# Optimization experiments

Measured on AMD Instinct MI355X. Metric: run time of the kernel, lower is better.

## Reference

```python
import jax, jax.numpy as jnp
import numpy as np
from jax import lax

PRE_NMS_THRESH = 0.05
PRE_NMS_TOP_N = 1000
FINAL_NMS_THRESH = 0.4  # hardcoded in forward(): boxlist_nms(..., 0.4)
MIN_SIZE = 0
STRIDE = 4.0
NEG = -1e9

N, C, H, W = 32, 1, 384, 384


def setup_inputs() -> dict:
    key = jax.random.key(0)
    k1, k2 = jax.random.split(key)
    box_cls = jax.random.uniform(k1, (N, C, H, W), dtype=jnp.float32)
    box_regression = jax.random.normal(k2, (N, 4, H, W), dtype=jnp.float32) * 20.0
    image_sizes = jnp.full((N, 2), H * int(STRIDE), dtype=jnp.int32)
    return {"box_cls": box_cls, "box_regression": box_regression, "image_sizes": image_sizes}


def decode_boxes(quad):
    # quad: [N, 4, H, W]; EAST geometry decode at stride 4 -> xyxy
    n, _, h, w = quad.shape
    x = (jnp.arange(w, dtype=quad.dtype) * STRIDE)[None, :]   # [1, W]
    y = (jnp.arange(h, dtype=quad.dtype) * STRIDE)[:, None]   # [H, 1]
    ymin = y - quad[:, 0]
    xmax = x + quad[:, 1]
    ymax = y + quad[:, 2]
    xmin = x - quad[:, 3]
    return jnp.stack([xmin, ymin, xmax, ymax], axis=1)  # [N, 4, H, W] (permute (3,0,1,2))


def iou_matrix(b):
    # b: [K, 4] xyxy
    x1, y1, x2, y2 = b[:, 0], b[:, 1], b[:, 2], b[:, 3]
    area = jnp.clip(x2 - x1, 0) * jnp.clip(y2 - y1, 0)
    ix1 = jnp.maximum(x1[:, None], x1[None, :])
    iy1 = jnp.maximum(y1[:, None], y1[None, :])
    ix2 = jnp.minimum(x2[:, None], x2[None, :])
    iy2 = jnp.minimum(y2[:, None], y2[None, :])
    inter = jnp.clip(ix2 - ix1, 0) * jnp.clip(iy2 - iy1, 0)
    union = area[:, None] + area[None, :] - inter
    return inter / jnp.maximum(union, 1e-9)


def greedy_nms(boxes, init_keep):
    # boxes: [K, 4] sorted by descending score; init_keep: [K] bool
    K = boxes.shape[0]
    iou = iou_matrix(boxes)
    idx = jnp.arange(K)

    def body(i, keep):
        suppress = (iou[i] > FINAL_NMS_THRESH) & (idx > i)
        return jnp.where(keep[i], keep & ~suppress, keep)

    return lax.fori_loop(0, K, body, init_keep)


def _forward(box_cls, box_regression):
    n, c, h, w = box_cls.shape
    boxes = decode_boxes(box_regression)                       # [N, 4, H, W]
    boxes = boxes.transpose(0, 2, 3, 1).reshape(n, h * w, 4)   # [N, HW, 4]
    scores = box_cls.transpose(0, 2, 3, 1).reshape(n, h * w)   # [N, HW] (C=1)

    # threshold + conditional top-k (padding with NEG emulates variable counts)
    masked = jnp.where(scores > PRE_NMS_THRESH, scores, NEG)
    scores_k, idx_k = lax.top_k(masked, PRE_NMS_TOP_N)         # [N, K], sorted desc
    boxes_k = jnp.take_along_axis(boxes, idx_k[..., None], axis=1)  # [N, K, 4]

    valid = scores_k > PRE_NMS_THRESH
    ws = boxes_k[..., 2] - boxes_k[..., 0]
    hs = boxes_k[..., 3] - boxes_k[..., 1]
    valid = valid & (ws >= MIN_SIZE) & (hs >= MIN_SIZE)        # remove_small_boxes

    keep = jax.vmap(greedy_nms)(boxes_k, valid)                # [N, K]
    out = jnp.concatenate([boxes_k, scores_k[..., None]], axis=-1)
    out = out * keep[..., None].astype(out.dtype)              # [N, K, 5]
    return out, keep


def reference(box_cls, box_regression, image_sizes):
    return _forward(box_cls, box_regression)
```

## Files before the change

kernel.cpp:

```cpp
#include <hip/hip_runtime.h>
#include <stdint.h>

#define NIMG 32
#define WID 384
#define HW 147456
#define TOPK 1000
#define KPAD 1024
#define NBINS 512
#define BIN_SCALEF 512.0f
#define SEGCAP 256
#define CANDCAP 2048
#define THRESH 0.05f
#define PREF_C 0.99f
#define NMS_T 0.4f
#define NBLK 18

typedef unsigned long long u64;
typedef unsigned int u32;

#define PCNT_OFF 0
#define PCAND_OFF 4096

__device__ __forceinline__ float area_of(float x0, float y0, float x1, float y1) {
  float a = fmaxf(x1 - x0, 0.0f) * fmaxf(y1 - y0, 0.0f);
  asm volatile("" : "+v"(a));
  return a;
}

__device__ __forceinline__ bool iou_gt(float ax0, float ay0, float ax1, float ay1, float aa,
                                       float bx0, float by0, float bx1, float by1, float ba) {
  float ix1 = fmaxf(ax0, bx0);
  float iy1 = fmaxf(ay0, by0);
  float ix2 = fminf(ax1, bx1);
  float iy2 = fminf(ay1, by1);
  float iw = fmaxf(ix2 - ix1, 0.0f);
  float ih = fmaxf(iy2 - iy1, 0.0f);
  float inter = iw * ih;
  asm volatile("" : "+v"(inter));
  float uni = fmaxf(aa + ba - inter, 1e-9f);
  return (inter / uni) > NMS_T;
}

__device__ __forceinline__ u64 shflxor64(u64 v, int m) {
  int lo = __shfl_xor((int)(u32)v, m, 64);
  int hi = __shfl_xor((int)(u32)(v >> 32), m, 64);
  return ((u64)(u32)hi << 32) | (u32)lo;
}

__device__ __forceinline__ u64 make_key(float s, u32 idx) {
  u32 ord = __float_as_uint(s) | 0x80000000u;
  return ((u64)ord << 32) | (u32)(~idx);
}

__device__ __forceinline__ int bin_of(float s) {
  int b = (int)(s * BIN_SCALEF);
  return b < 0 ? 0 : (b > NBINS - 1 ? NBINS - 1 : b);
}

__global__ __launch_bounds__(256) void scan_kernel(const float* __restrict__ cls,
                                                   u32* __restrict__ pcnt,
                                                   u64* __restrict__ pcand) {
  __shared__ u64 lbuf[SEGCAP];
  __shared__ u32 lcnt;
  const int n = blockIdx.y;
  const int tid = threadIdx.x;
  const int lane = tid & 63;
  if (tid == 0) lcnt = 0;
  __syncthreads();

  const float4* src = (const float4*)(cls + (size_t)n * HW) + blockIdx.x * 2048;
  float4 A[8];
#pragma unroll
  for (int v = 0; v < 8; v++) A[v] = src[tid + v * 256];

  const u64 ltmask = (1ull << lane) - 1ull;
#pragma unroll
  for (int v = 0; v < 8; v++) {
    float ss[4] = {A[v].x, A[v].y, A[v].z, A[v].w};
#pragma unroll
    for (int c = 0; c < 4; c++) {
      float s = ss[c];
      bool pc = s > PREF_C;
      u64 m = __ballot(pc);
      if (m) {
        int ldr = __ffsll(m) - 1;
        u32 wb = 0;
        if (lane == ldr) wb = atomicAdd(&lcnt, (u32)__popcll(m));
        wb = (u32)__shfl((int)wb, ldr, 64);
        if (pc) {
          u32 pos = wb + (u32)__popcll(m & ltmask);
          if (pos < SEGCAP) lbuf[pos] = make_key(s, (u32)((blockIdx.x * 2048 + tid + v * 256) * 4 + c));
        }
      }
    }
  }
  __syncthreads();
  const int seg = n * NBLK + blockIdx.x;
  if (tid == 0) pcnt[seg] = (lcnt > SEGCAP) ? 0xFFFFFFFFu : lcnt;
  u32 c = lcnt < SEGCAP ? lcnt : (u32)SEGCAP;
  u64* pc = pcand + (size_t)seg * SEGCAP;
  for (u32 i = tid; i < c; i += 256) pc[i] = lbuf[i];
}

#define REGCHAIN(K, JSTART) do {                                            \
    const bool desc_ = ((tid & ((K) >> 1)) == 0);                           \
    for (int j_ = (JSTART); j_ >= 2; j_ >>= 1) {                            \
      int h_ = j_ >> 1;                                                     \
      bool low_ = (tid & h_) == 0;                                          \
      u64 p0_ = shflxor64(e0, h_), p1_ = shflxor64(e1, h_);                 \
      bool tm_ = (low_ == desc_);                                           \
      e0 = tm_ ? (e0 > p0_ ? e0 : p0_) : (e0 < p0_ ? e0 : p0_);             \
      e1 = tm_ ? (e1 > p1_ ? e1 : p1_) : (e1 < p1_ ? e1 : p1_);             \
    }                                                                       \
    { u64 lo_ = e0 < e1 ? e0 : e1, hi_ = e0 < e1 ? e1 : e0;                 \
      e0 = desc_ ? hi_ : lo_; e1 = desc_ ? lo_ : hi_; }                     \
  } while (0)

__global__ __launch_bounds__(1024) void fused_kernel(const float* __restrict__ cls,
                                                     const float* __restrict__ reg,
                                                     const u32* __restrict__ pcnt,
                                                     const u64* __restrict__ pcand,
                                                     float* __restrict__ out) {
  __shared__ u64 skey[CANDCAP];
  __shared__ u32 scnt[NBLK];
  __shared__ u32 soff[NBLK];
  __shared__ u32 bs[NBINS];
  __shared__ u32 stmp[64];
  __shared__ int stbin;
  __shared__ u32 sflag, sfc;
  __shared__ float4 vbox[KPAD];
  __shared__ float varea[KPAD];
  __shared__ u64 mlds[136 * 64];
  __shared__ u32 wcnt[16], woff[16];
  __shared__ int pc[136], pk[136];
  __shared__ int sV, snch, snp;
  __shared__ u64 keepsh[16], srem[16];

  const int n = blockIdx.x;
  const int tid = threadIdx.x;
  const int lane = tid & 63;
  const u64 ltmask = (1ull << lane) - 1ull;

  if (tid < NBLK) scnt[tid] = pcnt[n * NBLK + tid];
  skey[tid] = 0ull; skey[tid + 1024] = 0ull;
  if (tid == 0) sfc = 0;
  __syncthreads();
  if (tid == 0) {
    u32 f = 0, off = 0;
    for (int s = 0; s < NBLK; s++) {
      u32 c = scnt[s];
      if (c == 0xFFFFFFFFu) { f = 1; c = 0; }
      soff[s] = off; off += c;
    }
    if (off < TOPK || off > CANDCAP) f = 1;
    sflag = f;
  }
  __syncthreads();

  if (sflag == 0) {
    for (int s = 0; s < NBLK; s++) {
      u32 c = scnt[s];
      if (tid < c) skey[soff[s] + tid] = pcand[(size_t)(n * NBLK + s) * SEGCAP + tid];
    }
  } else {
    for (int i = tid; i < NBINS; i += 1024) bs[i] = 0;
    __syncthreads();
    const float* ci = cls + (size_t)n * HW;
    for (int base = 0; base < HW; base += 1024) {
      float s = ci[base + tid];
      if (s > THRESH) atomicAdd(&bs[bin_of(s)], 1u);
    }
    __syncthreads();
    if (tid < 64) {
      u32 cs = 0;
#pragma unroll
      for (int k2 = 0; k2 < 8; k2++) cs += bs[lane * 8 + k2];
      u32 s = cs;
#pragma unroll
      for (int d = 1; d < 64; d <<= 1) {
        u32 v = (u32)__shfl_down((int)s, d, 64);
        if (lane + d < 64) s += v;
      }
      stmp[lane] = s;
      u64 mask = __ballot(s >= TOPK);
      if (lane == 0) {
        int t = 0;
        if (mask) {
          int L = 63 - __clzll(mask);
          u32 acc = (L < 63) ? stmp[L + 1] : 0;
          for (int b = L * 8 + 7; b >= L * 8; b--) {
            acc += bs[b];
            if (acc >= TOPK) { t = b; break; }
          }
        }
        stbin = t;
      }
    }
    __syncthreads();
    const int t = stbin;
    for (int base = 0; base < HW; base += 1024) {
      int i = base + tid;
      float s = ci[i];
      bool p = (s > THRESH) && (bin_of(s) >= t);
      u64 m = __ballot(p);
      if (m) {
        int ldr = __ffsll(m) - 1;
        u32 wb = 0;
        if (lane == ldr) wb = atomicAdd(&sfc, (u32)__popcll(m));
        wb = (u32)__shfl((int)wb, ldr, 64);
        if (p) { u32 pos = wb + (u32)__popcll(m & ltmask); if (pos < CANDCAP) skey[pos] = make_key(s, (u32)i); }
      }
    }
  }
  __syncthreads();

  {
    u64 e0 = skey[2 * tid], e1 = skey[2 * tid + 1];
    REGCHAIN(2, 1); REGCHAIN(4, 2); REGCHAIN(8, 4); REGCHAIN(16, 8);
    REGCHAIN(32, 16); REGCHAIN(64, 32); REGCHAIN(128, 64);
    for (int k = 256; k <= CANDCAP; k <<= 1) {
      skey[2 * tid] = e0; skey[2 * tid + 1] = e1;
      __syncthreads();
      for (int j = k >> 1; j >= 128; j >>= 1) {
        int i = ((tid & ~(j - 1)) << 1) | (tid & (j - 1));
        u64 a = skey[i], b = skey[i + j];
        bool desc = ((i & k) == 0);
        if (desc ? (a < b) : (a > b)) { skey[i] = b; skey[i + j] = a; }
        __syncthreads();
      }
      e0 = skey[2 * tid]; e1 = skey[2 * tid + 1];
      REGCHAIN(k, 64);
    }
    skey[2 * tid] = e0; skey[2 * tid + 1] = e1;
    __syncthreads();
  }

  u64 key = skey[tid];
  float4 b = make_float4(0.f, 0.f, 0.f, 0.f);
  if (key != 0ull && tid < TOPK) {
    u32 idx = ~(u32)(key & 0xFFFFFFFFull);
    int iy = (int)idx / WID;
    int ix = (int)idx - iy * WID;
    float xx = (float)ix * 4.0f;
    float yy = (float)iy * 4.0f;
    const float* rb = reg + (size_t)n * 4 * HW;
    float r0 = rb[idx];
    float r1 = rb[HW + idx];
    float r2 = rb[2 * HW + idx];
    float r3 = rb[3 * HW + idx];
    b.y = yy - r0; b.z = xx + r1; b.w = yy + r2; b.x = xx - r3;
  }
  float s = __uint_as_float((u32)(key >> 32) & 0x7FFFFFFFu);

  bool vb = (tid < TOPK) && (s > THRESH) && (b.z - b.x >= 0.0f) && (b.w - b.y >= 0.0f);
  vbox[tid] = make_float4(0.f, 0.f, 0.f, 0.f);
  varea[tid] = 0.0f;
  const int w = tid >> 6;
  u64 vm = __ballot(vb);
  if (lane == 0) wcnt[w] = (u32)__popcll(vm);
  if (tid < 16) { srem[tid] = 0ull; keepsh[tid] = 0ull; }
  __syncthreads();
  if (tid == 0) {
    u32 off = 0;
    for (int i = 0; i < 16; i++) { woff[i] = off; off += wcnt[i]; }
    int V = (int)off;
    int nch = (V + 63) >> 6;
    sV = V; snch = nch; snp = nch * (nch + 1) / 2;
  }
  __syncthreads();
  const int V = sV, nch = snch, npairs = snp;

  int pos = -1;
  if (vb) {
    pos = (int)(woff[w] + (u32)__popcll(vm & ltmask));
    vbox[pos] = b;
    varea[pos] = area_of(b.x, b.y, b.z, b.w);
  }
  if (tid < npairs) {
    int p = tid, c = 0, base = 0;
    while (p >= base + (nch - c)) { base += nch - c; c++; }
    pc[tid] = c; pk[tid] = c + (p - base);
  }
  __syncthreads();

  for (int r = w; r < npairs * 64; r += 16) {
    int p = r >> 6, i = r & 63;
    int c = pc[p], k = pk[p];
    float4 rbx = vbox[k * 64 + i];
    float rarea = varea[k * 64 + i];
    float4 cbx = vbox[c * 64 + lane];
    float carea = varea[c * 64 + lane];
    bool pred = iou_gt(rbx.x, rbx.y, rbx.z, rbx.w, rarea,
                       cbx.x, cbx.y, cbx.z, cbx.w, carea);
    u64 m = __ballot(pred);
    if (lane == 0) mlds[r] = m;
  }
  __syncthreads();

  if (tid < 64) {
    for (int c = 0; c < nch; c++) {
      int pbase = c * nch - (c * (c - 1)) / 2 - c;
      u64 diag = mlds[(pbase + c) * 64 + lane];
      u64 ainit = (V >= (c + 1) * 64) ? ~0ull
                : ((V > c * 64) ? ((1ull << (V - c * 64)) - 1ull) : 0ull);
      u64 alive;
      {
        u64 a = ainit & ~srem[c];
        u32 alo2 = __builtin_amdgcn_readfirstlane((u32)a);
        u32 ahi2 = __builtin_amdgcn_readfirstlane((u32)(a >> 32));
        alive = ((u64)ahi2 << 32) | alo2;
      }
      u32 rlo = (u32)diag, rhi = (u32)(diag >> 32);
      u64 cur = alive;
      while (cur) {
        int i = __ffsll(cur) - 1;
        u32 rl = __builtin_amdgcn_readlane(rlo, i);
        u32 rh = __builtin_amdgcn_readlane(rhi, i);
        u64 rowi = ((u64)rh << 32) | rl;
        u64 lowmask = (i == 63) ? ~0ull : ((1ull << (i + 1)) - 1ull);
        rowi &= ~lowmask;
        alive &= ~rowi;
        cur &= ~rowi;
        cur &= cur - 1;
      }
      if (lane == 0) keepsh[c] = alive;
      const u64 K = alive;
      for (int k = c + 1; k < nch; k++) {
        bool sup = (mlds[(pbase + k) * 64 + lane] & K) != 0ull;
        u64 mres = __ballot(sup);
        if (lane == 0) srem[k] |= mres;
      }
    }
  }
  __syncthreads();

  u64 kb = (vb && pos >= 0) ? ((keepsh[pos >> 6] >> (pos & 63)) & 1ull) : 0ull;
  if (tid < TOPK) {
    float f = (float)kb;
    size_t ob = (size_t)n * (TOPK * 5) + (size_t)tid * 5;
    out[ob + 0] = kb ? b.x : 0.0f;
    out[ob + 1] = kb ? b.y : 0.0f;
    out[ob + 2] = kb ? b.z : 0.0f;
    out[ob + 3] = kb ? b.w : 0.0f;
    out[ob + 4] = kb ? s : 0.0f;
    out[(size_t)NIMG * TOPK * 5 + (size_t)n * TOPK + tid] = f;
  }
}

extern "C" void kernel_launch(void* const* d_in, const int* in_sizes, int n_in,
                              void* d_out, int out_size, void* d_ws, size_t ws_size,
                              hipStream_t stream) {
  const float* cls = (const float*)d_in[0];
  const float* reg = (const float*)d_in[1];
  float* out = (float*)d_out;

  uint8_t* ws = (uint8_t*)d_ws;
  u32* pcnt = (u32*)(ws + PCNT_OFF);
  u64* pcand = (u64*)(ws + PCAND_OFF);

  scan_kernel<<<dim3(NBLK, NIMG), 256, 0, stream>>>(cls, pcnt, pcand);
  fused_kernel<<<NIMG, 1024, 0, stream>>>(cls, reg, pcnt, pcand, out);
}
```

Baseline: 177.8 us.

## Replace bitonic sort of candidates with fine-bin histogram rank sort

On the fast path, the full 2048-element bitonic sort of candidate keys is replaced by a fine histogram over scores in [0.99,1). Keys are bucketed, and each key's rank is computed by counting larger keys within its own bin. The key is then scattered directly to its rank position. Shared memory is unioned into one buffer reused by the later NMS stage. The bitonic sort is kept only for the fallback path, and an extra barrier is added to protect the aliased buffer.

```diff
diff --git a/kernel.cpp b/kernel.cpp
--- a/kernel.cpp
+++ b/kernel.cpp
@@ -14,6 +14,7 @@
 #define PREF_C 0.99f
 #define NMS_T 0.4f
 #define NBLK 18
+#define FINEBINS 256
 
 typedef unsigned long long u64;
 typedef unsigned int u32;
@@ -52,9 +53,19 @@
   return ((u64)ord << 32) | (u32)(~idx);
 }
 
+__device__ __forceinline__ float score_of(u64 key) {
+  return __uint_as_float((u32)(key >> 32) & 0x7FFFFFFFu);
+}
+
 __device__ __forceinline__ int bin_of(float s) {
   int b = (int)(s * BIN_SCALEF);
   return b < 0 ? 0 : (b > NBINS - 1 ? NBINS - 1 : b);
+}
+
+__device__ __forceinline__ int finebin(u64 key) {
+  float s = score_of(key);
+  int b = (int)((s - 0.99f) * 25600.0f);
+  return b < 0 ? 0 : (b > FINEBINS - 1 ? FINEBINS - 1 : b);
 }
 
 __global__ __launch_bounds__(256) void scan_kernel(const float* __restrict__ cls,
@@ -121,16 +132,23 @@
                                                      const u32* __restrict__ pcnt,
                                                      const u64* __restrict__ pcand,
                                                      float* __restrict__ out) {
-  __shared__ u64 skey[CANDCAP];
+  __shared__ __align__(16) unsigned char smem[90112];
+  u64* CKEY   = (u64*)smem;
+  u32* BINNED = (u32*)(smem + 16384);
+  u64* RKEY   = (u64*)(smem + 24576);
+  float4* vbox  = (float4*)smem;
+  float*  varea = (float*)(smem + 16384);
+  u64*    mlds  = (u64*)(smem + 20480);
+
+  __shared__ u32 BINSTART[FINEBINS + 1];
+  __shared__ u32 HIST[FINEBINS];
   __shared__ u32 scnt[NBLK];
   __shared__ u32 soff[NBLK];
   __shared__ u32 bs[NBINS];
   __shared__ u32 stmp[64];
   __shared__ int stbin;
   __shared__ u32 sflag, sfc;
-  __shared__ float4 vbox[KPAD];
-  __shared__ float varea[KPAD];
-  __shared__ u64 mlds[136 * 64];
+  __shared__ int sC;
   __shared__ u32 wcnt[16], woff[16];
   __shared__ int pc[136], pk[136];
   __shared__ int sV, snch, snp;
@@ -139,10 +157,13 @@
   const int n = blockIdx.x;
   const int tid = threadIdx.x;
   const int lane = tid & 63;
+  const int w = tid >> 6;
   const u64 ltmask = (1ull << lane) - 1ull;
 
   if (tid < NBLK) scnt[tid] = pcnt[n * NBLK + tid];
-  skey[tid] = 0ull; skey[tid + 1024] = 0ull;
+  CKEY[tid] = 0ull; CKEY[tid + 1024] = 0ull;
+  RKEY[tid] = 0ull;
+  if (tid < FINEBINS) HIST[tid] = 0;
   if (tid == 0) sfc = 0;
   __syncthreads();
   if (tid == 0) {
@@ -153,15 +174,63 @@
       soff[s] = off; off += c;
     }
     if (off < TOPK || off > CANDCAP) f = 1;
-    sflag = f;
-  }
-  __syncthreads();
+    sflag = f; sC = (int)off;
+  }
+  __syncthreads();
+
+  u64 key;
 
   if (sflag == 0) {
-    for (int s = 0; s < NBLK; s++) {
-      u32 c = scnt[s];
-      if (tid < c) skey[soff[s] + tid] = pcand[(size_t)(n * NBLK + s) * SEGCAP + tid];
-    }
+    const int C = sC;
+    for (int seg = w; seg < NBLK; seg += 16) {
+      u32 c = scnt[seg];
+      u32 o = soff[seg];
+      const u64* src2 = pcand + (size_t)(n * NBLK + seg) * SEGCAP;
+      for (u32 i = lane; i < c; i += 64) CKEY[o + i] = src2[i];
+    }
+    __syncthreads();
+    for (int i = tid; i < C; i += 1024) atomicAdd(&HIST[finebin(CKEY[i])], 1u);
+    __syncthreads();
+    if (tid < 64) {
+      u32 h0 = HIST[lane * 4 + 0], h1 = HIST[lane * 4 + 1];
+      u32 h2 = HIST[lane * 4 + 2], h3 = HIST[lane * 4 + 3];
+      u32 t = h0 + h1 + h2 + h3;
+      u32 incl = t;
+#pragma unroll
+      for (int d = 1; d < 64; d <<= 1) {
+        u32 v = (u32)__shfl_up((int)incl, d, 64);
+        if (lane >= d) incl += v;
+      }
+      u32 base = incl - t;
+      BINSTART[lane * 4 + 0] = base;
+      BINSTART[lane * 4 + 1] = base + h0;
+      BINSTART[lane * 4 + 2] = base + h0 + h1;
+      BINSTART[lane * 4 + 3] = base + h0 + h1 + h2;
+      if (lane == 63) BINSTART[FINEBINS] = incl;
+      HIST[lane * 4 + 0] = 0; HIST[lane * 4 + 1] = 0;
+      HIST[lane * 4 + 2] = 0; HIST[lane * 4 + 3] = 0;
+    }
+    __syncthreads();
+    for (int i = tid; i < C; i += 1024) {
+      int bb = finebin(CKEY[i]);
+      u32 slot = atomicAdd(&HIST[bb], 1u);
+      BINNED[BINSTART[bb] + slot] = (u32)i;
+    }
+    __syncthreads();
+    for (int i = tid; i < C; i += 1024) {
+      u64 k = CKEY[i];
+      int bb = finebin(k);
+      u32 s0 = BINSTART[bb], s1 = BINSTART[bb + 1];
+      u32 g = 0;
+      for (u32 j = s0; j < s1; j++) {
+        u32 cj = BINNED[j];
+        if (CKEY[cj] > k) g++;
+      }
+      u32 rank = (u32)C - s1 + g;
+      if (rank < KPAD) RKEY[rank] = k;
+    }
+    __syncthreads();
+    key = RKEY[tid];
   } else {
     for (int i = tid; i < NBINS; i += 1024) bs[i] = 0;
     __syncthreads();
@@ -188,9 +257,9 @@
         if (mask) {
           int L = 63 - __clzll(mask);
           u32 acc = (L < 63) ? stmp[L + 1] : 0;
-          for (int b = L * 8 + 7; b >= L * 8; b--) {
-            acc += bs[b];
-            if (acc >= TOPK) { t = b; break; }
+          for (int bb = L * 8 + 7; bb >= L * 8; bb--) {
+            acc += bs[bb];
+            if (acc >= TOPK) { t = bb; break; }
           }
         }
         stbin = t;
@@ -208,34 +277,33 @@
         u32 wb = 0;
         if (lane == ldr) wb = atomicAdd(&sfc, (u32)__popcll(m));
         wb = (u32)__shfl((int)wb, ldr, 64);
-        if (p) { u32 pos = wb + (u32)__popcll(m & ltmask); if (pos < CANDCAP) skey[pos] = make_key(s, (u32)i); }
-      }
-    }
-  }
-  __syncthreads();
-
-  {
-    u64 e0 = skey[2 * tid], e1 = skey[2 * tid + 1];
-    REGCHAIN(2, 1); REGCHAIN(4, 2); REGCHAIN(8, 4); REGCHAIN(16, 8);
-    REGCHAIN(32, 16); REGCHAIN(64, 32); REGCHAIN(128, 64);
-    for (int k = 256; k <= CANDCAP; k <<= 1) {
-      skey[2 * tid] = e0; skey[2 * tid + 1] = e1;
+        if (p) { u32 pos = wb + (u32)__popcll(m & ltmask); if (pos < CANDCAP) CKEY[pos] = make_key(s, (u32)i); }
+      }
+    }
+    __syncthreads();
+    {
+      u64 e0 = CKEY[2 * tid], e1 = CKEY[2 * tid + 1];
+      REGCHAIN(2, 1); REGCHAIN(4, 2); REGCHAIN(8, 4); REGCHAIN(16, 8);
+      REGCHAIN(32, 16); REGCHAIN(64, 32); REGCHAIN(128, 64);
+      for (int k = 256; k <= CANDCAP; k <<= 1) {
+        CKEY[2 * tid] = e0; CKEY[2 * tid + 1] = e1;
+        __syncthreads();
+        for (int j = k >> 1; j >= 128; j >>= 1) {
+          int i = ((tid & ~(j - 1)) << 1) | (tid & (j - 1));
+          u64 a = CKEY[i], bb = CKEY[i + j];
+          bool desc = ((i & k) == 0);
+          if (desc ? (a < bb) : (a > bb)) { CKEY[i] = bb; CKEY[i + j] = a; }
+          __syncthreads();
+        }
+        e0 = CKEY[2 * tid]; e1 = CKEY[2 * tid + 1];
+        REGCHAIN(k, 64);
+      }
+      CKEY[2 * tid] = e0; CKEY[2 * tid + 1] = e1;
       __syncthreads();
-      for (int j = k >> 1; j >= 128; j >>= 1) {
-        int i = ((tid & ~(j - 1)) << 1) | (tid & (j - 1));
-        u64 a = skey[i], b = skey[i + j];
-        bool desc = ((i & k) == 0);
-        if (desc ? (a < b) : (a > b)) { skey[i] = b; skey[i + j] = a; }
-        __syncthreads();
-      }
-      e0 = skey[2 * tid]; e1 = skey[2 * tid + 1];
-      REGCHAIN(k, 64);
-    }
-    skey[2 * tid] = e0; skey[2 * tid + 1] = e1;
-    __syncthreads();
-  }
-
-  u64 key = skey[tid];
+    }
+    key = CKEY[tid];
+  }
+
   float4 b = make_float4(0.f, 0.f, 0.f, 0.f);
   if (key != 0ull && tid < TOPK) {
     u32 idx = ~(u32)(key & 0xFFFFFFFFull);
@@ -250,12 +318,12 @@
     float r3 = rb[3 * HW + idx];
     b.y = yy - r0; b.z = xx + r1; b.w = yy + r2; b.x = xx - r3;
   }
-  float s = __uint_as_float((u32)(key >> 32) & 0x7FFFFFFFu);
+  float s = score_of(key);
+  __syncthreads();
 
   bool vb = (tid < TOPK) && (s > THRESH) && (b.z - b.x >= 0.0f) && (b.w - b.y >= 0.0f);
   vbox[tid] = make_float4(0.f, 0.f, 0.f, 0.f);
   varea[tid] = 0.0f;
-  const int w = tid >> 6;
   u64 vm = __ballot(vb);
   if (lane == 0) wcnt[w] = (u32)__popcll(vm);
   if (tid < 16) { srem[tid] = 0ull; keepsh[tid] = 0ull; }
```

Measured after the change: 165.2 us. -7.1%, faster.
